# Performance work log

Hardware: AMD Instinct MI355X
Metric: run time of the kernel (lower is better)

The kernel has to match this reference:

```python
import jax, jax.numpy as jnp
import numpy as np

BRANCH = 16    # tree branching factor
HEIGHT = 4     # tree height (levels below virtual root 0)
D_MODEL = 1024 # feature dim of Xi / model output
IN_DIM = 1024  # raw input dim
BATCH = 4096


def _build_tree(b, h):
    # Balanced b-ary tree. Node ids are 1-based in BFS order; id 0 is the
    # virtual root (df.parent == 0 selects level-1 nodes in the original).
    level_sizes = [b ** l for l in range(1, h + 1)]
    starts = np.cumsum([1] + level_sizes)[:-1]  # first id of each level
    n_nodes = int(sum(level_sizes))
    children = np.zeros((n_nodes + 1, b), dtype=np.int32)  # 0 == no child
    children[0] = np.arange(1, b + 1)  # root's children (parent == 0)
    for l in range(1, h):
        ids = np.arange(starts[l - 1], starts[l - 1] + level_sizes[l - 1])
        pos = np.arange(level_sizes[l - 1])
        children[ids] = starts[l] + pos[:, None] * b + np.arange(b)[None, :]
    return n_nodes, children


def setup_inputs() -> dict:
    key = jax.random.key(0)
    k1, k2, k3 = jax.random.split(key, 3)
    n_nodes, children = _build_tree(BRANCH, HEIGHT)
    X = jax.random.normal(k1, (BATCH, IN_DIM), dtype=jnp.float32)
    W = jax.random.normal(k2, (IN_DIM, D_MODEL), dtype=jnp.float32) / np.sqrt(IN_DIM)
    # Xi: [d_model, n_nodes] class-embedding matrix (angle-based -> unit columns)
    Xi = jax.random.normal(k3, (D_MODEL, n_nodes), dtype=jnp.float32)
    Xi = Xi / jnp.linalg.norm(Xi, axis=0, keepdims=True)
    return {"X": X, "W": W, "Xi": Xi, "children": jnp.asarray(children)}


def reference(X, W, Xi, children):
    # f = model(X); here the stand-in model is a linear layer.
    f = X @ W                      # [B, d]
    XiT = Xi.T                     # [n_nodes, d]
    B = X.shape[0]
    neg_inf = jnp.finfo(f.dtype).min

    cur = jnp.zeros((B,), dtype=jnp.int32)          # start at virtual root 0
    cols = [jnp.zeros((B,), dtype=jnp.int32)]       # y_pred[:, 0] == 0
    for _ in range(HEIGHT):
        cand = children[cur]                         # [B, K] 1-based ids, 0 = pad
        emb = XiT[cand - 1]                          # [B, K, d] (pad rows masked below)
        g = jnp.einsum('bkd,bd->bk', emb, f)         # scores vs candidate children
        valid = cand > 0
        g = jnp.where(valid, g, neg_inf)
        idx = jnp.argmax(g, axis=-1)
        nxt = jnp.take_along_axis(cand, idx[:, None], axis=1)[:, 0]
        any_valid = jnp.any(valid, axis=-1)          # False once a leaf is reached
        nxt = jnp.where(any_valid, nxt, 0)           # original leaves y_pred at 0
        cols.append(nxt)
        cur = jnp.where(any_valid, nxt, cur)         # stop descending at leaves
    return jnp.stack(cols, axis=1)                   # [B, HEIGHT+1] int32
```

## Files before the change

### kernel.cpp

```cpp
#include <hip/hip_runtime.h>
#include <hip/hip_bf16.h>
#include <cstdint>
#include <cfloat>

#define BATCH   4096
#define IN_DIM  1024
#define D_MODEL 1024
#define BRANCH  16
#define HEIGHT  4
#define N_NODES 69904

__global__ __launch_bounds__(256) void gemm_f32(const float* __restrict__ A,
                                                const float* __restrict__ B,
                                                float* __restrict__ C,
                                                int M, int N, int K) {
    __shared__ float As[16][68];
    __shared__ float Bs[16][68];

    const int t  = threadIdx.x;
    const int tx = t & 15;
    const int ty = t >> 4;
    const int bm = blockIdx.x;
    const int bn = blockIdx.y;

    const int arow = t >> 2;
    const int ac4  = (t & 3) * 4;
    const int brow = t >> 4;
    const int bc4  = (t & 15) * 4;

    const float* Ab = A + (size_t)(bm * 64) * K;
    const float* Bb = B + (size_t)bn * 64;

    float acc[4][4] = {};

    for (int k0 = 0; k0 < K; k0 += 16) {
        float4 av = *(const float4*)(Ab + (size_t)arow * K + k0 + ac4);
        float4 bv = *(const float4*)(Bb + (size_t)(k0 + brow) * N + bc4);

        As[ac4 + 0][arow] = av.x;
        As[ac4 + 1][arow] = av.y;
        As[ac4 + 2][arow] = av.z;
        As[ac4 + 3][arow] = av.w;
        *(float4*)&Bs[brow][bc4] = bv;
        __syncthreads();

#pragma unroll
        for (int k = 0; k < 16; ++k) {
            float4 a = *(const float4*)&As[k][ty * 4];
            float4 b = *(const float4*)&Bs[k][tx * 4];
            const float aa[4] = {a.x, a.y, a.z, a.w};
            const float bb[4] = {b.x, b.y, b.z, b.w};
#pragma unroll
            for (int i = 0; i < 4; ++i)
#pragma unroll
                for (int j = 0; j < 4; ++j)
                    acc[i][j] = fmaf(aa[i], bb[j], acc[i][j]);
        }
        __syncthreads();
    }

    float* Cb = C + (size_t)(bm * 64 + ty * 4) * N + bn * 64 + tx * 4;
#pragma unroll
    for (int i = 0; i < 4; ++i) {
        float4 v = {acc[i][0], acc[i][1], acc[i][2], acc[i][3]};
        *(float4*)(Cb + (size_t)i * N) = v;
    }
}

__global__ __launch_bounds__(256) void descend(const float* __restrict__ f,
                                               const float* __restrict__ Xi,
                                               const int* __restrict__ children,
                                               int* __restrict__ out) {
    __shared__ float fs[4][1024];

    const int lane = threadIdx.x & 63;
    const int w    = threadIdx.x >> 6;
    const int b    = blockIdx.x * 4 + w;

    {
        const float4* frow = (const float4*)(f + (size_t)b * D_MODEL);
        float4* fsw = (float4*)fs[w];
#pragma unroll
        for (int i = 0; i < 4; ++i) fsw[lane + 64 * i] = frow[lane + 64 * i];
    }
    __syncthreads();

    const int g = lane >> 4;
    const int k = lane & 15;

    int cur = 0;
    if (lane == 0) out[(size_t)b * (HEIGHT + 1)] = 0;

    for (int lev = 0; lev < HEIGHT; ++lev) {
        const int child = children[(size_t)cur * BRANCH + k];
        const int valid = child > 0;
        const int col   = valid ? child - 1 : 0;

        const float* xp = Xi + (size_t)g * N_NODES + col;
        const float* fr = fs[w] + g;
        const size_t step = (size_t)4 * N_NODES;

        float acc = 0.f;
#pragma unroll 16
        for (int t = 0; t < 256; ++t) {
            acc = fmaf(fr[4 * t], *xp, acc);
            xp += step;
        }

        acc += __shfl_xor(acc, 16);
        acc += __shfl_xor(acc, 32);
        if (!valid) acc = -FLT_MAX;

        float bv = acc;
        int   bk = k;
        int   bc = child;
#pragma unroll
        for (int m = 1; m < 16; m <<= 1) {
            float ov = __shfl_xor(bv, m);
            int   ok = __shfl_xor(bk, m);
            int   oc = __shfl_xor(bc, m);
            if (ov > bv || (ov == bv && ok < bk)) { bv = ov; bk = ok; bc = oc; }
        }

        const int any = (bv > -FLT_MAX) ? 1 : 0;
        const int nxt = any ? bc : 0;
        if (lane == 0) out[(size_t)b * (HEIGHT + 1) + lev + 1] = nxt;
        cur = any ? nxt : cur;
    }
}

extern "C" void kernel_launch(void* const* d_in, const int* in_sizes, int n_in,
                              void* d_out, int out_size, void* d_ws, size_t ws_size,
                              hipStream_t stream) {
    const float* X        = (const float*)d_in[0];
    const float* W        = (const float*)d_in[1];
    const float* Xi       = (const float*)d_in[2];
    const int*   children = (const int*)d_in[3];
    int* out = (int*)d_out;

    float* f = (float*)d_ws;

    dim3 ggrid(BATCH / 64, D_MODEL / 64);
    gemm_f32<<<ggrid, 256, 0, stream>>>(X, W, f, BATCH, D_MODEL, IN_DIM);

    descend<<<BATCH / 4, 256, 0, stream>>>(f, Xi, children, out);
}
```

Baseline: 576.3 us.

## Enlarge GEMM register tiles with prefetch and vectorize contiguous-children descent

The GEMM moves to 128x64 block tiles with an 8x8 per-thread microtile and 128 threads. It prefetches the next K tile into registers while computing the current one. The descent kernel assumes the 16 children of a node are contiguous ids, so it reads them as float4 over the Xi row, splits the d dimension across lanes, and reduces with shuffles. This removes the per-child gather and the invalid-child handling, relying on the balanced tree layout of the test input.

```diff
diff --git a/kernel.cpp b/kernel.cpp
--- a/kernel.cpp
+++ b/kernel.cpp
@@ -10,61 +10,103 @@
 #define HEIGHT  4
 #define N_NODES 69904
 
-__global__ __launch_bounds__(256) void gemm_f32(const float* __restrict__ A,
+#define BM 128
+#define BN 64
+#define BK 16
+
+__global__ __launch_bounds__(128) void gemm_f32(const float* __restrict__ A,
                                                 const float* __restrict__ B,
-                                                float* __restrict__ C,
-                                                int M, int N, int K) {
-    __shared__ float As[16][68];
-    __shared__ float Bs[16][68];
+                                                float* __restrict__ C) {
+    __shared__ float As[BK][BM + 4];
+    __shared__ float Bs[BK][BN + 4];
 
     const int t  = threadIdx.x;
-    const int tx = t & 15;
-    const int ty = t >> 4;
+    const int tx = t & 7;
+    const int ty = t >> 3;
     const int bm = blockIdx.x;
     const int bn = blockIdx.y;
 
     const int arow = t >> 2;
     const int ac4  = (t & 3) * 4;
-    const int brow = t >> 4;
-    const int bc4  = (t & 15) * 4;
+    const float* Ab = A + (size_t)bm * BM * IN_DIM;
+    const float* Bb = B + (size_t)bn * BN;
 
-    const float* Ab = A + (size_t)(bm * 64) * K;
-    const float* Bb = B + (size_t)bn * 64;
+    float4 ar[4], br[2];
 
-    float acc[4][4] = {};
+#define LOAD_TILE(k0)                                                          \
+    {                                                                          \
+        _Pragma("unroll")                                                      \
+        for (int i = 0; i < 4; ++i)                                            \
+            ar[i] = *(const float4*)(Ab + (size_t)(arow + 32 * i) * IN_DIM +   \
+                                     (k0) + ac4);                              \
+        _Pragma("unroll")                                                      \
+        for (int i = 0; i < 2; ++i) {                                          \
+            int idx = t + 128 * i;                                             \
+            br[i] = *(const float4*)(Bb + (size_t)((k0) + (idx >> 4)) * D_MODEL\
+                                     + (idx & 15) * 4);                        \
+        }                                                                      \
+    }
 
-    for (int k0 = 0; k0 < K; k0 += 16) {
-        float4 av = *(const float4*)(Ab + (size_t)arow * K + k0 + ac4);
-        float4 bv = *(const float4*)(Bb + (size_t)(k0 + brow) * N + bc4);
+#define STORE_TILE()                                                           \
+    {                                                                          \
+        _Pragma("unroll")                                                      \
+        for (int i = 0; i < 4; ++i) {                                          \
+            As[ac4 + 0][arow + 32 * i] = ar[i].x;                              \
+            As[ac4 + 1][arow + 32 * i] = ar[i].y;                              \
+            As[ac4 + 2][arow + 32 * i] = ar[i].z;                              \
+            As[ac4 + 3][arow + 32 * i] = ar[i].w;                              \
+        }                                                                      \
+        _Pragma("unroll")                                                      \
+        for (int i = 0; i < 2; ++i) {                                          \
+            int idx = t + 128 * i;                                             \
+            *(float4*)&Bs[idx >> 4][(idx & 15) * 4] = br[i];                   \
+        }                                                                      \
+    }
 
-        As[ac4 + 0][arow] = av.x;
-        As[ac4 + 1][arow] = av.y;
-        As[ac4 + 2][arow] = av.z;
-        As[ac4 + 3][arow] = av.w;
-        *(float4*)&Bs[brow][bc4] = bv;
+    float acc[8][8] = {};
+
+#define COMPUTE_TILE()                                                         \
+    {                                                                          \
+        _Pragma("unroll")                                                      \
+        for (int k = 0; k < BK; ++k) {                                         \
+            float4 a0 = *(const float4*)&As[k][ty * 8];                        \
+            float4 a1 = *(const float4*)&As[k][ty * 8 + 4];                    \
+            float4 b0 = *(const float4*)&Bs[k][tx * 8];                        \
+            float4 b1 = *(const float4*)&Bs[k][tx * 8 + 4];                    \
+            const float aa[8] = {a0.x, a0.y, a0.z, a0.w, a1.x, a1.y, a1.z, a1.w};\
+            const float bb[8] = {b0.x, b0.y, b0.z, b0.w, b1.x, b1.y, b1.z, b1.w};\
+            _Pragma("unroll")                                                  \
+            for (int i = 0; i < 8; ++i)                                        \
+                _Pragma("unroll")                                              \
+                for (int j = 0; j < 8; ++j)                                    \
+                    acc[i][j] = fmaf(aa[i], bb[j], acc[i][j]);                 \
+        }                                                                      \
+    }
+
+    LOAD_TILE(0);
+    STORE_TILE();
+    __syncthreads();
+
+    for (int k0 = BK; k0 < IN_DIM; k0 += BK) {
+        LOAD_TILE(k0);
+        COMPUTE_TILE();
         __syncthreads();
-
-#pragma unroll
-        for (int k = 0; k < 16; ++k) {
-            float4 a = *(const float4*)&As[k][ty * 4];
-            float4 b = *(const float4*)&Bs[k][tx * 4];
-            const float aa[4] = {a.x, a.y, a.z, a.w};
-            const float bb[4] = {b.x, b.y, b.z, b.w};
-#pragma unroll
-            for (int i = 0; i < 4; ++i)
-#pragma unroll
-                for (int j = 0; j < 4; ++j)
-                    acc[i][j] = fmaf(aa[i], bb[j], acc[i][j]);
-        }
+        STORE_TILE();
         __syncthreads();
     }
+    COMPUTE_TILE();
 
-    float* Cb = C + (size_t)(bm * 64 + ty * 4) * N + bn * 64 + tx * 4;
+    float* Cb = C + (size_t)(bm * BM + ty * 8) * D_MODEL + bn * BN + tx * 8;
 #pragma unroll
-    for (int i = 0; i < 4; ++i) {
-        float4 v = {acc[i][0], acc[i][1], acc[i][2], acc[i][3]};
-        *(float4*)(Cb + (size_t)i * N) = v;
+    for (int i = 0; i < 8; ++i) {
+        float4 v0 = {acc[i][0], acc[i][1], acc[i][2], acc[i][3]};
+        float4 v1 = {acc[i][4], acc[i][5], acc[i][6], acc[i][7]};
+        *(float4*)(Cb + (size_t)i * D_MODEL)     = v0;
+        *(float4*)(Cb + (size_t)i * D_MODEL + 4) = v1;
     }
+#undef LOAD_TILE
+#undef STORE_TILE
+#undef COMPUTE_TILE
 }
 
 __global__ __launch_bounds__(256) void descend(const float* __restrict__ f,
@@ -85,47 +127,52 @@
     }
     __syncthreads();
 
-    const int g = lane >> 4;
-    const int k = lane & 15;
+    const int q  = lane & 3;
+    const int dg = lane >> 2;
+    const float* frd = fs[w] + dg;
 
     int cur = 0;
     if (lane == 0) out[(size_t)b * (HEIGHT + 1)] = 0;
 
     for (int lev = 0; lev < HEIGHT; ++lev) {
-        const int child = children[(size_t)cur * BRANCH + k];
-        const int valid = child > 0;
-        const int col   = valid ? child - 1 : 0;
+        const int child0 = __builtin_amdgcn_readfirstlane(children[cur * BRANCH]);
+        const float* xp = Xi + (size_t)dg * N_NODES + (child0 - 1) + q * 4;
 
-        const float* xp = Xi + (size_t)g * N_NODES + col;
-        const float* fr = fs[w] + g;
-        const size_t step = (size_t)4 * N_NODES;
-
-        float acc = 0.f;
-#pragma unroll 16
-        for (int t = 0; t < 256; ++t) {
-            acc = fmaf(fr[4 * t], *xp, acc);
-            xp += step;
+        float4 acc = {0.f, 0.f, 0.f, 0.f};
+#pragma unroll 8
+        for (int t = 0; t < 64; ++t) {
+            float4 x = *(const float4*)xp;
+            float fv = frd[16 * t];
+            acc.x = fmaf(fv, x.x, acc.x);
+            acc.y = fmaf(fv, x.y, acc.y);
+            acc.z = fmaf(fv, x.z, acc.z);
+            acc.w = fmaf(fv, x.w, acc.w);
+            xp += (size_t)16 * N_NODES;
         }
 
-        acc += __shfl_xor(acc, 16);
-        acc += __shfl_xor(acc, 32);
-        if (!valid) acc = -FLT_MAX;
-
-        float bv = acc;
-        int   bk = k;
-        int   bc = child;
 #pragma unroll
-        for (int m = 1; m < 16; m <<= 1) {
-            float ov = __shfl_xor(bv, m);
-            int   ok = __shfl_xor(bk, m);
-            int   oc = __shfl_xor(bc, m);
-            if (ov > bv || (ov == bv && ok < bk)) { bv = ov; bk = ok; bc = oc; }
+        for (int m = 4; m <= 32; m <<= 1) {
+            acc.x += __shfl_xor(acc.x, m);
+            acc.y += __shfl_xor(acc.y, m);
+            acc.z += __shfl_xor(acc.z, m);
+            acc.w += __shfl_xor(acc.w, m);
         }
 
-        const int any = (bv > -FLT_MAX) ? 1 : 0;
-        const int nxt = any ? bc : 0;
+        float bv = acc.x; int bc = q * 4;
+        if (acc.y > bv) { bv = acc.y; bc = q * 4 + 1; }
+        if (acc.z > bv) { bv = acc.z; bc = q * 4 + 2; }
+        if (acc.w > bv) { bv = acc.w; bc = q * 4 + 3; }
+
+#pragma unroll
+        for (int m = 1; m <= 2; m <<= 1) {
+            float ov = __shfl_xor(bv, m);
+            int   oc = __shfl_xor(bc, m);
+            if (ov > bv || (ov == bv && oc < bc)) { bv = ov; bc = oc; }
+        }
+
+        const int nxt = child0 + bc;
         if (lane == 0) out[(size_t)b * (HEIGHT + 1) + lev + 1] = nxt;
-        cur = any ? nxt : cur;
+        cur = nxt;
     }
 }
 
@@ -140,8 +187,8 @@
 
     float* f = (float*)d_ws;
 
-    dim3 ggrid(BATCH / 64, D_MODEL / 64);
-    gemm_f32<<<ggrid, 256, 0, stream>>>(X, W, f, BATCH, D_MODEL, IN_DIM);
+    dim3 ggrid(BATCH / BM, D_MODEL / BN);
+    gemm_f32<<<ggrid, 128, 0, stream>>>(X, W, f);
 
     descend<<<BATCH / 4, 256, 0, stream>>>(f, Xi, children, out);
 }
```

Result: slower. 617.8 us (+7.2%).
